# Kernel tuning notes

Hardware: AMD Instinct MI355X
Metric: run time of the kernel (lower is better)

The kernel has to match this reference:

```python
import jax, jax.numpy as jnp
import numpy as np

ITERATIONS = 3
EPS = 1e-06

def squash(s):
    # square_norm along last dim, keepdims (matches torch squash)
    sq = jnp.sum(s * s, axis=-1, keepdims=True)
    return sq / (1.0 + sq) * s / (jnp.sqrt(sq) + EPS)

def setup_inputs() -> dict:
    key = jax.random.key(0)
    k1, k2 = jax.random.split(key)
    x = jax.random.normal(k1, (64, 32, 8, 8, 16), dtype=jnp.float32)
    W = jax.random.normal(k2, (1, 32, 8, 8, 32, 16, 32), dtype=jnp.float32)
    return {"x": x, "W": W}

def reference(x, W):
    # u_hat: (B, C, H, Wd, O, D) = x (B,C,H,Wd,I) @ W (C,H,Wd,O,I,D)
    u_hat = jnp.einsum('bchwi,chwoid->bchwod', x, W[0])
    b = jnp.zeros(u_hat.shape[:-1], dtype=u_hat.dtype)  # (B,C,H,Wd,O)
    for _ in range(ITERATIONS - 1):
        c = jax.nn.softmax(b, axis=-1)
        s = jnp.sum(c[..., None] * u_hat, axis=(1, 2, 3))  # (B,O,D)
        v = squash(s)
        b = b + jnp.sum(u_hat * v[:, None, None, None], axis=-1)
    c = jax.nn.softmax(b, axis=-1)
    s = jnp.sum(c[..., None] * u_hat, axis=(1, 2, 3))
    return squash(s)  # (B, out_capsules, out_cap_dim)
```

## Files before the change

kernel.cpp:

```cpp
#include <hip/hip_runtime.h>
#include <math.h>

#define B_ 64
#define N_ 2048
#define O_ 32
#define I_ 16
#define D_ 32
#define OD_ 1024

typedef __attribute__((ext_vector_type(8))) short bf16x8;
typedef __attribute__((ext_vector_type(4))) float f32x4;

union FragU { unsigned u[4]; uint4 v; bf16x8 f; };

__device__ __forceinline__ void barrier_lds() {
  asm volatile("s_waitcnt lgkmcnt(0)\n\ts_barrier" ::: "memory");
}

template <int CTRL>
__device__ __forceinline__ float dpp_mov_f(float x) {
  return __int_as_float(
      __builtin_amdgcn_update_dpp(0, __float_as_int(x), CTRL, 0xf, 0xf, true));
}
__device__ __forceinline__ float grp32_max(float x) {
  x = fmaxf(x, dpp_mov_f<0xb1>(x));
  x = fmaxf(x, dpp_mov_f<0x4e>(x));
  x = fmaxf(x, dpp_mov_f<0x124>(x));
  x = fmaxf(x, dpp_mov_f<0x128>(x));
  x = fmaxf(x, __shfl_xor(x, 16));
  return x;
}
__device__ __forceinline__ float grp32_sum(float x) {
  x += dpp_mov_f<0xb1>(x);
  x += dpp_mov_f<0x4e>(x);
  x += dpp_mov_f<0x124>(x);
  x += dpp_mov_f<0x128>(x);
  x += __shfl_xor(x, 16);
  return x;
}

__device__ __forceinline__ void dk_split(float f, unsigned &h, unsigned &l) {
  unsigned u = __float_as_uint(f);
  h = u & 0xffff0000u;
  float lo = f - __uint_as_float(h);
  l = __float_as_uint(lo) >> 16;
}
__device__ __forceinline__ void dk_split16(float f, unsigned short &h,
                                           unsigned short &l) {
  unsigned u = __float_as_uint(f);
  unsigned hu = u & 0xffff0000u;
  h = (unsigned short)(u >> 16);
  float lo = f - __uint_as_float(hu);
  l = (unsigned short)(__float_as_uint(lo) >> 16);
}
__device__ __forceinline__ unsigned pk(unsigned short e0, unsigned short e1) {
  return (unsigned)e0 | ((unsigned)e1 << 16);
}

__global__ __launch_bounds__(256) void prep_all(const float* __restrict__ W,
                                                const float* __restrict__ x,
                                                uint4* __restrict__ WP,
                                                uint4* __restrict__ XP) {
  __shared__ float tile[8 * 512];
  const int tid = threadIdx.x;
  if (blockIdx.x < 8192) {
    const int pair0 = blockIdx.x * 8;
    const f32x4* gsrc = (const f32x4*)(W + (size_t)pair0 * 512);
    f32x4* lds4 = (f32x4*)tile;
#pragma unroll
    for (int k = 0; k < 4; ++k)
      lds4[tid + k * 256] = __builtin_nontemporal_load(gsrc + tid + k * 256);
    __syncthreads();
    const int p = tid >> 5;
    const int d = tid & 31;
    const int pair = pair0 + p;
    unsigned short hh[I_], ll[I_];
#pragma unroll
    for (int i = 0; i < I_; ++i)
      dk_split16(tile[p * 512 + i * 32 + d], hh[i], ll[i]);
    const int c = d & 15, dhalf = d >> 4;
    size_t base = ((size_t)pair * 2 + dhalf) * 4;
#pragma unroll
    for (int sel = 0; sel < 2; ++sel) {
      const unsigned short* e = sel ? ll : hh;
#pragma unroll
      for (int qp = 0; qp < 2; ++qp) {
        uint4 u;
        u.x = pk(e[qp * 8 + 0], e[qp * 8 + 1]);
        u.y = pk(e[qp * 8 + 2], e[qp * 8 + 3]);
        u.z = pk(e[qp * 8 + 4], e[qp * 8 + 5]);
        u.w = pk(e[qp * 8 + 6], e[qp * 8 + 7]);
        WP[(base + sel * 2 + qp) * 16 + c] = u;
      }
    }
  } else {
    int t = (blockIdx.x - 8192) * 256 + tid;
    int c = t & 15, n = (t >> 4) & 2047, bg = t >> 15;
    const f32x4* xq = (const f32x4*)(x + ((size_t)(bg * 16 + c) * N_ + n) * I_);
    float xv[I_];
#pragma unroll
    for (int k = 0; k < 4; ++k) {
      f32x4 q4 = __builtin_nontemporal_load(xq + k);
      xv[4 * k + 0] = q4[0];
      xv[4 * k + 1] = q4[1];
      xv[4 * k + 2] = q4[2];
      xv[4 * k + 3] = q4[3];
    }
    unsigned short hh[I_], ll[I_];
#pragma unroll
    for (int i = 0; i < I_; ++i) dk_split16(xv[i], hh[i], ll[i]);
    size_t base = ((size_t)bg * N_ + n) * 4;
#pragma unroll
    for (int sel = 0; sel < 2; ++sel) {
      const unsigned short* e = sel ? ll : hh;
#pragma unroll
      for (int qp = 0; qp < 2; ++qp) {
        uint4 u;
        u.x = pk(e[qp * 8 + 0], e[qp * 8 + 1]);
        u.y = pk(e[qp * 8 + 2], e[qp * 8 + 3]);
        u.z = pk(e[qp * 8 + 4], e[qp * 8 + 5]);
        u.w = pk(e[qp * 8 + 6], e[qp * 8 + 7]);
        XP[(base + sel * 2 + qp) * 16 + c] = u;
      }
    }
  }
}

template <int UNIFORM>
__global__ __launch_bounds__(1024, 4) void mfma_pass6(
    const uint4* __restrict__ XP, const uint4* __restrict__ WP,
    const float* __restrict__ v, float* __restrict__ partial, int NC) {
  const int tid = threadIdx.x;
  const int lane = tid & 63;
  const int w = tid >> 6;
  const int q = lane >> 4;
  const int c = lane & 15;
  const int qp = q & 1;
  const int ch = blockIdx.x;
  const int bgy = blockIdx.y;

  __shared__ uint4 xps[2][16][4][16];
  __shared__ float ls_l[32 * 33];
  __shared__ float ls_c2[32 * 33];

  const int n0 = ch * NC;

  {
    uint4* xf = (uint4*)xps;
    const int total = 2 * NC * 64;
    for (int l = tid; l < total; l += 1024) {
      int bgl = l / (NC * 64);
      int rest = l - bgl * (NC * 64);
      xf[bgl * 1024 + rest] =
          XP[(size_t)(bgy * 2 + bgl) * 131072 + (size_t)n0 * 64 + rest];
    }
  }

  f32x4 s_t[2][4];
#pragma unroll
  for (int bgl = 0; bgl < 2; ++bgl)
#pragma unroll
    for (int ct = 0; ct < 4; ++ct) s_t[bgl][ct] = (f32x4){0.f, 0.f, 0.f, 0.f};

  float vreg[2][4][4];
  if (!UNIFORM) {
#pragma unroll
    for (int bgl = 0; bgl < 2; ++bgl)
#pragma unroll
      for (int ct = 0; ct < 4; ++ct) {
        const float4 vv = *(const float4*)&v[(size_t)(bgy * 32 + bgl * 16 + c) * OD_ +
                                             (2 * w + (ct >> 1)) * 32 +
                                             (ct & 1) * 16 + q * 4];
        vreg[bgl][ct][0] = vv.x;
        vreg[bgl][ct][1] = vv.y;
        vreg[bgl][ct][2] = vv.z;
        vreg[bgl][ct][3] = vv.w;
      }
  }

  barrier_lds();

  const uint4* wbase = WP + (size_t)(2 * w) * 128 + lane;

  FragU cb[4];
#pragma unroll
  for (int ct = 0; ct < 4; ++ct)
    cb[ct].v = wbase[(size_t)n0 * 4096 + ct * 64];

  if (UNIFORM) {
    for (int nl = 0; nl < NC; ++nl) {
      const size_t n = (size_t)(n0 + nl);
      const size_t np = (nl + 1 < NC) ? n + 1 : n;
      FragU cbn[4];
#pragma unroll
      for (int ct = 0; ct < 4; ++ct) cbn[ct].v = wbase[np * 4096 + ct * 64];
#pragma unroll
      for (int bgl = 0; bgl < 2; ++bgl) {
        FragU ah, al;
        ah.v = xps[bgl][nl][qp][c];
        al.v = xps[bgl][nl][2 + qp][c];
#pragma unroll
        for (int ct = 0; ct < 4; ++ct) {
          s_t[bgl][ct] = __builtin_amdgcn_mfma_f32_16x16x32_bf16(
              ah.f, cb[ct].f, s_t[bgl][ct], 0, 0, 0);
          s_t[bgl][ct] = __builtin_amdgcn_mfma_f32_16x16x32_bf16(
              al.f, cb[ct].f, s_t[bgl][ct], 0, 0, 0);
        }
      }
#pragma unroll
      for (int ct = 0; ct < 4; ++ct) cb[ct] = cbn[ct];
    }
  } else {
    for (int nl = 0; nl < NC; ++nl) {
      const size_t n = (size_t)(n0 + nl);
      const size_t np = (nl + 1 < NC) ? n + 1 : n;

      f32x4 ut[2][4];
#pragma unroll
      for (int bgl = 0; bgl < 2; ++bgl) {
        FragU ah, al;
        ah.v = xps[bgl][nl][qp][c];
        al.v = xps[bgl][nl][2 + qp][c];
        float lgol[2] = {0.f, 0.f};
#pragma unroll
        for (int ct = 0; ct < 4; ++ct) {
          f32x4 accT = (f32x4){0.f, 0.f, 0.f, 0.f};
          accT = __builtin_amdgcn_mfma_f32_16x16x32_bf16(cb[ct].f, ah.f, accT, 0, 0, 0);
          ut[bgl][ct] = __builtin_amdgcn_mfma_f32_16x16x32_bf16(cb[ct].f, al.f, accT, 0, 0, 0);
          const int ol = ct >> 1;
#pragma unroll
          for (int r = 0; r < 4; ++r)
            lgol[ol] = fmaf(ut[bgl][ct][r], vreg[bgl][ct][r], lgol[ol]);
        }
#pragma unroll
        for (int ol = 0; ol < 2; ++ol) {
          float t = lgol[ol];
          t += __shfl_xor(t, 16);
          t += __shfl_xor(t, 32);
          if (q == 0) ls_l[(2 * w + ol) * 33 + bgl * 16 + c] = t;
        }
      }
#pragma unroll
      for (int ct = 0; ct < 4; ++ct) cb[ct].v = wbase[np * 4096 + ct * 64];

      barrier_lds();
      {
        const int idx = (tid & 31) * 33 + (tid >> 5);
        float l = ls_l[idx];
        float mx = grp32_max(l);
        float e = __expf(l - mx);
        float sm = grp32_sum(e);
        ls_c2[idx] = e / sm;
      }
      barrier_lds();
#pragma unroll
      for (int bgl = 0; bgl < 2; ++bgl)
#pragma unroll
        for (int ol = 0; ol < 2; ++ol) {
          const float cc = ls_c2[(2 * w + ol) * 33 + bgl * 16 + c];
#pragma unroll
          for (int dh = 0; dh < 2; ++dh) {
            const int ct = ol * 2 + dh;
#pragma unroll
            for (int r = 0; r < 4; ++r)
              s_t[bgl][ct][r] = fmaf(cc, ut[bgl][ct][r], s_t[bgl][ct][r]);
          }
        }
    }
  }

  if (UNIFORM) {
    const float scale = 1.f / 32.f;
#pragma unroll
    for (int bgl = 0; bgl < 2; ++bgl)
#pragma unroll
      for (int ct = 0; ct < 4; ++ct) {
        int odc = (2 * w + (ct >> 1)) * 32 + (ct & 1) * 16 + c;
#pragma unroll
        for (int r = 0; r < 4; ++r) {
          partial[((size_t)ch * B_ + bgy * 32 + bgl * 16 + q * 4 + r) * OD_ + odc] =
              s_t[bgl][ct][r] * scale;
        }
      }
  } else {
    float* tw = ((float*)xps) + w * 288;
#pragma unroll
    for (int bgl = 0; bgl < 2; ++bgl)
#pragma unroll
      for (int ct = 0; ct < 4; ++ct) {
#pragma unroll
        for (int r = 0; r < 4; ++r) tw[c * 18 + q * 4 + r] = s_t[bgl][ct][r];
        f32x4 so;
#pragma unroll
        for (int r = 0; r < 4; ++r) so[r] = tw[(q * 4 + r) * 18 + c];
        const int odc = (2 * w + (ct >> 1)) * 32 + (ct & 1) * 16 + c;
#pragma unroll
        for (int r = 0; r < 4; ++r) {
          partial[((size_t)ch * B_ + bgy * 32 + bgl * 16 + q * 4 + r) * OD_ + odc] =
              so[r];
        }
      }
  }
}

template <int UNIFORM>
__global__ __launch_bounds__(512, 4) void mfma_pass_fb(
    const float* __restrict__ x, const float* __restrict__ W,
    const float* __restrict__ v, float* __restrict__ partial, int NC) {
  const int tid = threadIdx.x;
  const int lane = tid & 63;
  const int cg = tid >> 6;
  const int q = lane >> 4;
  const int c = lane & 15;
  const int ch = blockIdx.x;
  const int bg = blockIdx.y;

  __shared__ float ls_logit[16 * O_];
  __shared__ float ls_c[16 * O_];

  f32x4 s_t[8];
#pragma unroll
  for (int ct = 0; ct < 8; ++ct) s_t[ct] = (f32x4){0.f, 0.f, 0.f, 0.f};

  const int n0 = ch * NC;
  const int ih = (q & 1) * 8;
  const float* xrow = x + ((size_t)(bg * 16 + c) * N_) * I_ + ih;

  for (int nl = 0; nl < NC; ++nl) {
    const int n = n0 + nl;
    const float* xp = xrow + (size_t)n * I_;
    float4 xv0 = *(const float4*)xp;
    float4 xv1 = *(const float4*)(xp + 4);
    float xv[8] = {xv0.x, xv0.y, xv0.z, xv0.w, xv1.x, xv1.y, xv1.z, xv1.w};
    FragU a1;
#pragma unroll
    for (int p = 0; p < 4; ++p) {
      unsigned h0, l0, h1, l1;
      dk_split(xv[2 * p], h0, l0);
      dk_split(xv[2 * p + 1], h1, l1);
      a1.u[p] = (q < 2) ? ((h0 >> 16) | h1) : (l0 | (l1 << 16));
    }
    f32x4 u_t[8];
#pragma unroll
    for (int ct = 0; ct < 8; ++ct) {
      const int o = cg * 4 + (ct >> 1);
      const int d = (ct & 1) * 16 + c;
      const float* wp = W + (((size_t)n * O_ + o) * I_ + ih) * D_ + d;
      FragU b1, b2;
#pragma unroll
      for (int p = 0; p < 4; ++p) {
        unsigned h0, l0, h1, l1;
        dk_split(wp[(2 * p) * D_], h0, l0);
        dk_split(wp[(2 * p + 1) * D_], h1, l1);
        b1.u[p] = (h0 >> 16) | h1;
        b2.u[p] = l0 | (l1 << 16);
      }
      if (UNIFORM) {
        s_t[ct] = __builtin_amdgcn_mfma_f32_16x16x32_bf16(a1.f, b1.f, s_t[ct], 0, 0, 0);
        s_t[ct] = __builtin_amdgcn_mfma_f32_16x16x32_bf16(a1.f, b2.f, s_t[ct], 0, 0, 0);
      } else {
        f32x4 acc = (f32x4){0.f, 0.f, 0.f, 0.f};
        acc = __builtin_amdgcn_mfma_f32_16x16x32_bf16(a1.f, b1.f, acc, 0, 0, 0);
        u_t[ct] = __builtin_amdgcn_mfma_f32_16x16x32_bf16(a1.f, b2.f, acc, 0, 0, 0);
      }
    }
    if (!UNIFORM) {
#pragma unroll
      for (int ol = 0; ol < 4; ++ol) {
        float lg[4] = {0.f, 0.f, 0.f, 0.f};
#pragma unroll
        for (int hf = 0; hf < 2; ++hf) {
          int ct = ol * 2 + hf;
          int odc = cg * 128 + ct * 16 + c;
#pragma unroll
          for (int r = 0; r < 4; ++r)
            lg[r] = fmaf(u_t[ct][r], v[(size_t)(bg * 16 + q * 4 + r) * OD_ + odc], lg[r]);
        }
#pragma unroll
        for (int r = 0; r < 4; ++r) {
#pragma unroll
          for (int m = 1; m < 16; m <<= 1) lg[r] += __shfl_xor(lg[r], m);
        }
        if (c == 0) {
#pragma unroll
          for (int r = 0; r < 4; ++r)
            ls_logit[(q * 4 + r) * O_ + cg * 4 + ol] = lg[r];
        }
      }
      __syncthreads();
      {
        int b_l = tid >> 5, o = tid & 31;
        float l = ls_logit[b_l * O_ + o];
        float mx = l;
#pragma unroll
        for (int m = 16; m >= 1; m >>= 1) mx = fmaxf(mx, __shfl_xor(mx, m));
        float e = __expf(l - mx);
        float sm = e;
#pragma unroll
        for (int m = 16; m >= 1; m >>= 1) sm += __shfl_xor(sm, m);
        ls_c[b_l * O_ + o] = e / sm;
      }
      __syncthreads();
#pragma unroll
      for (int ol = 0; ol < 4; ++ol) {
        int o = cg * 4 + ol;
        float cc[4];
#pragma unroll
        for (int r = 0; r < 4; ++r) cc[r] = ls_c[(q * 4 + r) * O_ + o];
#pragma unroll
        for (int hf = 0; hf < 2; ++hf) {
          int ct = ol * 2 + hf;
#pragma unroll
          for (int r = 0; r < 4; ++r)
            s_t[ct][r] = fmaf(cc[r], u_t[ct][r], s_t[ct][r]);
        }
      }
    }
  }

  const float scale = UNIFORM ? (1.f / 32.f) : 1.f;
#pragma unroll
  for (int ct = 0; ct < 8; ++ct) {
#pragma unroll
    for (int r = 0; r < 4; ++r) {
      partial[((size_t)ch * B_ + bg * 16 + q * 4 + r) * OD_ + cg * 128 + ct * 16 + c] =
          s_t[ct][r] * scale;
    }
  }
}

__global__ __launch_bounds__(256) void reduce_fused(
    const float4* __restrict__ part, int cq4, const float4* __restrict__ prev,
    float4* __restrict__ out) {
  __shared__ float4 accs[4][64];
  const int lane = threadIdx.x & 63;
  const int cg = threadIdx.x >> 6;
  const int g4 = blockIdx.x * 64 + lane;
  float4 s = make_float4(0.f, 0.f, 0.f, 0.f);
  const int c0 = cg * cq4;
  for (int i = 0; i < cq4; ++i) {
    float4 p = part[(size_t)(c0 + i) * 16384 + g4];
    s.x += p.x; s.y += p.y; s.z += p.z; s.w += p.w;
  }
  accs[cg][lane] = s;
  __syncthreads();
  if (cg == 0) {
    float4 a1 = accs[1][lane], a2 = accs[2][lane], a3 = accs[3][lane];
    s.x += a1.x + a2.x + a3.x;
    s.y += a1.y + a2.y + a3.y;
    s.z += a1.z + a2.z + a3.z;
    s.w += a1.w + a2.w + a3.w;
    float sq = s.x * s.x + s.y * s.y + s.z * s.z + s.w * s.w;
#pragma unroll
    for (int m = 4; m >= 1; m >>= 1) sq += __shfl_xor(sq, m, 8);
    float scale = sq / ((1.f + sq) * (sqrtf(sq) + 1e-6f));
    float4 r = make_float4(s.x * scale, s.y * scale, s.z * scale, s.w * scale);
    if (prev) {
      float4 p = prev[g4];
      r.x += p.x; r.y += p.y; r.z += p.z; r.w += p.w;
    }
    out[g4] = r;
  }
}

__global__ __launch_bounds__(256) void reduce_squash(
    const float4* __restrict__ part, int chunks,
    const float4* __restrict__ prev, float4* __restrict__ out) {
  int g4 = blockIdx.x * 256 + threadIdx.x;
  float4 s = make_float4(0.f, 0.f, 0.f, 0.f);
#pragma unroll 4
  for (int ch = 0; ch < chunks; ++ch) {
    float4 p = part[(size_t)ch * 16384 + g4];
    s.x += p.x; s.y += p.y; s.z += p.z; s.w += p.w;
  }
  float sq = s.x * s.x + s.y * s.y + s.z * s.z + s.w * s.w;
#pragma unroll
  for (int m = 4; m >= 1; m >>= 1) sq += __shfl_xor(sq, m, 8);
  float scale = sq / ((1.f + sq) * (sqrtf(sq) + 1e-6f));
  float4 r = make_float4(s.x * scale, s.y * scale, s.z * scale, s.w * scale);
  if (prev) {
    float4 p = prev[g4];
    r.x += p.x; r.y += p.y; r.z += p.z; r.w += p.w;
  }
  out[g4] = r;
}

extern "C" void kernel_launch(void* const* d_in, const int* in_sizes, int n_in,
                              void* d_out, int out_size, void* d_ws,
                              size_t ws_size, hipStream_t stream) {
  const float* x = (const float*)d_in[0];
  const float* W = (const float*)d_in[1];
  float* out = (float*)d_out;

  const size_t XP_FLOATS = 4ull * 2048 * 4 * 16 * 4;
  const size_t WP_FLOATS = 2048ull * 32 * 2 * 4 * 16 * 4;

  float* v1 = (float*)d_ws;
  float* vsum = v1 + 65536;
  float* partial = vsum + 65536;

  const int chunks = 128;
  bool packed_path =
      (131072 + (size_t)chunks * 65536 + XP_FLOATS + WP_FLOATS) * 4 <= ws_size;

  if (packed_path) {
    uint4* XP = (uint4*)(partial + (size_t)chunks * 65536);
    uint4* WP = XP + XP_FLOATS / 4;
    const int NC = N_ / chunks;
    const int cq4 = chunks / 4;
    dim3 grid(chunks, 2);

    prep_all<<<8704, 256, 0, stream>>>(W, x, WP, XP);

    mfma_pass6<1><<<grid, 1024, 0, stream>>>(XP, WP, nullptr, partial, NC);
    reduce_fused<<<256, 256, 0, stream>>>((const float4*)partial, cq4, nullptr,
                                          (float4*)v1);
    mfma_pass6<0><<<grid, 1024, 0, stream>>>(XP, WP, v1, partial, NC);
    reduce_fused<<<256, 256, 0, stream>>>((const float4*)partial, cq4,
                                          (const float4*)v1, (float4*)vsum);
    mfma_pass6<0><<<grid, 1024, 0, stream>>>(XP, WP, vsum, partial, NC);
    reduce_fused<<<256, 256, 0, stream>>>((const float4*)partial, cq4, nullptr,
                                          (float4*)out);
  } else {
    int fchunks = 128;
    while (fchunks > 1 && (131072 + (size_t)fchunks * 65536) * 4 > ws_size)
      fchunks >>= 1;
    int NC = N_ / fchunks;
    dim3 grid(fchunks, 4);

    mfma_pass_fb<1><<<grid, 512, 0, stream>>>(x, W, nullptr, partial, NC);
    reduce_squash<<<64, 256, 0, stream>>>((const float4*)partial, fchunks,
                                          nullptr, (float4*)v1);
    mfma_pass_fb<0><<<grid, 512, 0, stream>>>(x, W, v1, partial, NC);
    reduce_squash<<<64, 256, 0, stream>>>((const float4*)partial, fchunks,
                                          (const float4*)v1, (float4*)vsum);
    mfma_pass_fb<0><<<grid, 512, 0, stream>>>(x, W, vsum, partial, NC);
    reduce_squash<<<64, 256, 0, stream>>>((const float4*)partial, fchunks,
                                          nullptr, (float4*)out);
  }
}
```

Before: 355.4 us.

## Split routing pass into uniform kernel and narrower 512-thread non-uniform kernel

Splits the templated pass into a dedicated uniform-routing kernel and a separate non-uniform kernel. In the non-uniform kernel each block now handles one 16-batch group with 512 threads (grid doubled in y), and each wave covers four output capsules instead of two. The v vector is now loaded from global memory every iteration through an opaque offset rather than held in registers, which lowers register pressure. The aim is more blocks and smaller barriers in the softmax-per-step loop. The cost is that each W fragment is fetched twice as often across blocks, plus extra v loads inside the loop.

```diff
diff --git a/kernel.cpp b/kernel.cpp
--- a/kernel.cpp
+++ b/kernel.cpp
@@ -126,8 +126,84 @@
   }
 }
 
-template <int UNIFORM>
-__global__ __launch_bounds__(1024, 4) void mfma_pass6(
+__global__ __launch_bounds__(1024, 4) void mfma_pass_u(
+    const uint4* __restrict__ XP, const uint4* __restrict__ WP,
+    float* __restrict__ partial, int NC) {
+  const int tid = threadIdx.x;
+  const int lane = tid & 63;
+  const int w = tid >> 6;
+  const int q = lane >> 4;
+  const int c = lane & 15;
+  const int qp = q & 1;
+  const int ch = blockIdx.x;
+  const int bgy = blockIdx.y;
+
+  __shared__ uint4 xps[2][16][4][16];
+
+  const int n0 = ch * NC;
+  {
+    uint4* xf = (uint4*)xps;
+    const int total = 2 * NC * 64;
+    for (int l = tid; l < total; l += 1024) {
+      int bgl = l / (NC * 64);
+      int rest = l - bgl * (NC * 64);
+      xf[bgl * 1024 + rest] =
+          XP[(size_t)(bgy * 2 + bgl) * 131072 + (size_t)n0 * 64 + rest];
+    }
+  }
+
+  f32x4 s_t[2][4];
+#pragma unroll
+  for (int bgl = 0; bgl < 2; ++bgl)
+#pragma unroll
+    for (int ct = 0; ct < 4; ++ct) s_t[bgl][ct] = (f32x4){0.f, 0.f, 0.f, 0.f};
+
+  barrier_lds();
+
+  const uint4* wbase = WP + (size_t)(2 * w) * 128 + lane;
+  FragU cb[4];
+#pragma unroll
+  for (int ct = 0; ct < 4; ++ct)
+    cb[ct].v = wbase[(size_t)n0 * 4096 + ct * 64];
+
+  for (int nl = 0; nl < NC; ++nl) {
+    const size_t n = (size_t)(n0 + nl);
+    const size_t np = (nl + 1 < NC) ? n + 1 : n;
+    FragU cbn[4];
+#pragma unroll
+    for (int ct = 0; ct < 4; ++ct) cbn[ct].v = wbase[np * 4096 + ct * 64];
+#pragma unroll
+    for (int bgl = 0; bgl < 2; ++bgl) {
+      FragU ah, al;
+      ah.v = xps[bgl][nl][qp][c];
+      al.v = xps[bgl][nl][2 + qp][c];
+#pragma unroll
+      for (int ct = 0; ct < 4; ++ct) {
+        s_t[bgl][ct] = __builtin_amdgcn_mfma_f32_16x16x32_bf16(
+            ah.f, cb[ct].f, s_t[bgl][ct], 0, 0, 0);
+        s_t[bgl][ct] = __builtin_amdgcn_mfma_f32_16x16x32_bf16(
+            al.f, cb[ct].f, s_t[bgl][ct], 0, 0, 0);
+      }
+    }
+#pragma unroll
+    for (int ct = 0; ct < 4; ++ct) cb[ct] = cbn[ct];
+  }
+
+  const float scale = 1.f / 32.f;
+#pragma unroll
+  for (int bgl = 0; bgl < 2; ++bgl)
+#pragma unroll
+    for (int ct = 0; ct < 4; ++ct) {
+      int odc = (2 * w + (ct >> 1)) * 32 + (ct & 1) * 16 + c;
+#pragma unroll
+      for (int r = 0; r < 4; ++r) {
+        partial[((size_t)ch * B_ + bgy * 32 + bgl * 16 + q * 4 + r) * OD_ + odc] =
+            s_t[bgl][ct][r] * scale;
+      }
+    }
+}
+
+__global__ __launch_bounds__(512, 4) void mfma_passN(
     const uint4* __restrict__ XP, const uint4* __restrict__ WP,
     const float* __restrict__ v, float* __restrict__ partial, int NC) {
   const int tid = threadIdx.x;
@@ -139,167 +215,106 @@
   const int ch = blockIdx.x;
   const int bgy = blockIdx.y;
 
-  __shared__ uint4 xps[2][16][4][16];
-  __shared__ float ls_l[32 * 33];
-  __shared__ float ls_c2[32 * 33];
+  __shared__ uint4 xps[16][4][16];
+  __shared__ float ls_l[32 * 17];
+  __shared__ float ls_c2[32 * 17];
 
   const int n0 = ch * NC;
 
   {
     uint4* xf = (uint4*)xps;
-    const int total = 2 * NC * 64;
-    for (int l = tid; l < total; l += 1024) {
-      int bgl = l / (NC * 64);
-      int rest = l - bgl * (NC * 64);
-      xf[bgl * 1024 + rest] =
-          XP[(size_t)(bgy * 2 + bgl) * 131072 + (size_t)n0 * 64 + rest];
-    }
-  }
-
-  f32x4 s_t[2][4];
-#pragma unroll
-  for (int bgl = 0; bgl < 2; ++bgl)
-#pragma unroll
-    for (int ct = 0; ct < 4; ++ct) s_t[bgl][ct] = (f32x4){0.f, 0.f, 0.f, 0.f};
-
-  float vreg[2][4][4];
-  if (!UNIFORM) {
-#pragma unroll
-    for (int bgl = 0; bgl < 2; ++bgl)
-#pragma unroll
-      for (int ct = 0; ct < 4; ++ct) {
-        const float4 vv = *(const float4*)&v[(size_t)(bgy * 32 + bgl * 16 + c) * OD_ +
-                                             (2 * w + (ct >> 1)) * 32 +
-                                             (ct & 1) * 16 + q * 4];
-        vreg[bgl][ct][0] = vv.x;
-        vreg[bgl][ct][1] = vv.y;
-        vreg[bgl][ct][2] = vv.z;
-        vreg[bgl][ct][3] = vv.w;
-      }
-  }
+    const int total = NC * 64;
+    for (int l = tid; l < total; l += 512)
+      xf[l] = XP[(size_t)bgy * 131072 + (size_t)n0 * 64 + l];
+  }
+
+  f32x4 s_t[8];
+#pragma unroll
+  for (int ct = 0; ct < 8; ++ct) s_t[ct] = (f32x4){0.f, 0.f, 0.f, 0.f};
 
   barrier_lds();
 
-  const uint4* wbase = WP + (size_t)(2 * w) * 128 + lane;
-
-  FragU cb[4];
-#pragma unroll
-  for (int ct = 0; ct < 4; ++ct)
-    cb[ct].v = wbase[(size_t)n0 * 4096 + ct * 64];
-
-  if (UNIFORM) {
-    for (int nl = 0; nl < NC; ++nl) {
-      const size_t n = (size_t)(n0 + nl);
-      const size_t np = (nl + 1 < NC) ? n + 1 : n;
-      FragU cbn[4];
-#pragma unroll
-      for (int ct = 0; ct < 4; ++ct) cbn[ct].v = wbase[np * 4096 + ct * 64];
-#pragma unroll
-      for (int bgl = 0; bgl < 2; ++bgl) {
-        FragU ah, al;
-        ah.v = xps[bgl][nl][qp][c];
-        al.v = xps[bgl][nl][2 + qp][c];
-#pragma unroll
-        for (int ct = 0; ct < 4; ++ct) {
-          s_t[bgl][ct] = __builtin_amdgcn_mfma_f32_16x16x32_bf16(
-              ah.f, cb[ct].f, s_t[bgl][ct], 0, 0, 0);
-          s_t[bgl][ct] = __builtin_amdgcn_mfma_f32_16x16x32_bf16(
-              al.f, cb[ct].f, s_t[bgl][ct], 0, 0, 0);
-        }
-      }
-#pragma unroll
-      for (int ct = 0; ct < 4; ++ct) cb[ct] = cbn[ct];
-    }
-  } else {
-    for (int nl = 0; nl < NC; ++nl) {
-      const size_t n = (size_t)(n0 + nl);
-      const size_t np = (nl + 1 < NC) ? n + 1 : n;
-
-      f32x4 ut[2][4];
-#pragma unroll
-      for (int bgl = 0; bgl < 2; ++bgl) {
-        FragU ah, al;
-        ah.v = xps[bgl][nl][qp][c];
-        al.v = xps[bgl][nl][2 + qp][c];
-        float lgol[2] = {0.f, 0.f};
-#pragma unroll
-        for (int ct = 0; ct < 4; ++ct) {
-          f32x4 accT = (f32x4){0.f, 0.f, 0.f, 0.f};
-          accT = __builtin_amdgcn_mfma_f32_16x16x32_bf16(cb[ct].f, ah.f, accT, 0, 0, 0);
-          ut[bgl][ct] = __builtin_amdgcn_mfma_f32_16x16x32_bf16(cb[ct].f, al.f, accT, 0, 0, 0);
-          const int ol = ct >> 1;
-#pragma unroll
-          for (int r = 0; r < 4; ++r)
-            lgol[ol] = fmaf(ut[bgl][ct][r], vreg[bgl][ct][r], lgol[ol]);
-        }
-#pragma unroll
-        for (int ol = 0; ol < 2; ++ol) {
-          float t = lgol[ol];
-          t += __shfl_xor(t, 16);
-          t += __shfl_xor(t, 32);
-          if (q == 0) ls_l[(2 * w + ol) * 33 + bgl * 16 + c] = t;
-        }
-      }
-#pragma unroll
-      for (int ct = 0; ct < 4; ++ct) cb[ct].v = wbase[np * 4096 + ct * 64];
-
-      barrier_lds();
-      {
-        const int idx = (tid & 31) * 33 + (tid >> 5);
-        float l = ls_l[idx];
-        float mx = grp32_max(l);
-        float e = __expf(l - mx);
-        float sm = grp32_sum(e);
-        ls_c2[idx] = e / sm;
-      }
-      barrier_lds();
-#pragma unroll
-      for (int bgl = 0; bgl < 2; ++bgl)
-#pragma unroll
-        for (int ol = 0; ol < 2; ++ol) {
-          const float cc = ls_c2[(2 * w + ol) * 33 + bgl * 16 + c];
-#pragma unroll
-          for (int dh = 0; dh < 2; ++dh) {
-            const int ct = ol * 2 + dh;
-#pragma unroll
-            for (int r = 0; r < 4; ++r)
-              s_t[bgl][ct][r] = fmaf(cc, ut[bgl][ct][r], s_t[bgl][ct][r]);
-          }
-        }
-    }
-  }
-
-  if (UNIFORM) {
-    const float scale = 1.f / 32.f;
-#pragma unroll
-    for (int bgl = 0; bgl < 2; ++bgl)
-#pragma unroll
-      for (int ct = 0; ct < 4; ++ct) {
-        int odc = (2 * w + (ct >> 1)) * 32 + (ct & 1) * 16 + c;
-#pragma unroll
-        for (int r = 0; r < 4; ++r) {
-          partial[((size_t)ch * B_ + bgy * 32 + bgl * 16 + q * 4 + r) * OD_ + odc] =
-              s_t[bgl][ct][r] * scale;
-        }
-      }
-  } else {
-    float* tw = ((float*)xps) + w * 288;
-#pragma unroll
-    for (int bgl = 0; bgl < 2; ++bgl)
-#pragma unroll
-      for (int ct = 0; ct < 4; ++ct) {
-#pragma unroll
-        for (int r = 0; r < 4; ++r) tw[c * 18 + q * 4 + r] = s_t[bgl][ct][r];
-        f32x4 so;
-#pragma unroll
-        for (int r = 0; r < 4; ++r) so[r] = tw[(q * 4 + r) * 18 + c];
-        const int odc = (2 * w + (ct >> 1)) * 32 + (ct & 1) * 16 + c;
-#pragma unroll
-        for (int r = 0; r < 4; ++r) {
-          partial[((size_t)ch * B_ + bgy * 32 + bgl * 16 + q * 4 + r) * OD_ + odc] =
-              so[r];
-        }
-      }
+  const uint4* wbase = WP + (size_t)(4 * w) * 128 + lane;
+  FragU cb[8];
+#pragma unroll
+  for (int ct = 0; ct < 8; ++ct)
+    cb[ct].v = wbase[(size_t)n0 * 4096 + (ct >> 1) * 128 + (ct & 1) * 64];
+
+  int zero = 0;
+  const size_t vrow = (size_t)(bgy * 16 + c) * OD_ + (4 * w) * 32 + q * 4;
+
+  for (int nl = 0; nl < NC; ++nl) {
+    const size_t n = (size_t)(n0 + nl);
+    const size_t np = (nl + 1 < NC) ? n + 1 : n;
+
+    asm volatile("" : "+v"(zero));
+    const float* vp = v + vrow + zero;
+
+    f32x4 ut[8];
+    FragU ah, al;
+    ah.v = xps[nl][qp][c];
+    al.v = xps[nl][2 + qp][c];
+    float lgol[4] = {0.f, 0.f, 0.f, 0.f};
+#pragma unroll
+    for (int ct = 0; ct < 8; ++ct) {
+      f32x4 accT = (f32x4){0.f, 0.f, 0.f, 0.f};
+      accT = __builtin_amdgcn_mfma_f32_16x16x32_bf16(cb[ct].f, ah.f, accT, 0, 0, 0);
+      ut[ct] = __builtin_amdgcn_mfma_f32_16x16x32_bf16(cb[ct].f, al.f, accT, 0, 0, 0);
+      const float4 vv =
+          *(const float4*)(vp + (ct >> 1) * 32 + (ct & 1) * 16);
+      const int ol = ct >> 1;
+      lgol[ol] = fmaf(ut[ct][0], vv.x, lgol[ol]);
+      lgol[ol] = fmaf(ut[ct][1], vv.y, lgol[ol]);
+      lgol[ol] = fmaf(ut[ct][2], vv.z, lgol[ol]);
+      lgol[ol] = fmaf(ut[ct][3], vv.w, lgol[ol]);
+    }
+#pragma unroll
+    for (int ol = 0; ol < 4; ++ol) {
+      float t = lgol[ol];
+      t += __shfl_xor(t, 16);
+      t += __shfl_xor(t, 32);
+      if (q == 0) ls_l[(4 * w + ol) * 17 + c] = t;
+    }
+#pragma unroll
+    for (int ct = 0; ct < 8; ++ct)
+      cb[ct].v = wbase[np * 4096 + (ct >> 1) * 128 + (ct & 1) * 64];
+
+    barrier_lds();
+    {
+      const int idx = (tid & 31) * 17 + (tid >> 5);
+      float l = ls_l[idx];
+      float mx = grp32_max(l);
+      float e = __expf(l - mx);
+      float sm = grp32_sum(e);
+      ls_c2[idx] = e / sm;
+    }
+    barrier_lds();
+#pragma unroll
+    for (int ol = 0; ol < 4; ++ol) {
+      const float cc = ls_c2[(4 * w + ol) * 17 + c];
+#pragma unroll
+      for (int dh = 0; dh < 2; ++dh) {
+        const int ct = ol * 2 + dh;
+#pragma unroll
+        for (int r = 0; r < 4; ++r)
+          s_t[ct][r] = fmaf(cc, ut[ct][r], s_t[ct][r]);
+      }
+    }
+  }
+
+  float* tw = ((float*)xps) + w * 288;
+#pragma unroll
+  for (int ct = 0; ct < 8; ++ct) {
+#pragma unroll
+    for (int r = 0; r < 4; ++r) tw[c * 18 + q * 4 + r] = s_t[ct][r];
+    f32x4 so;
+#pragma unroll
+    for (int r = 0; r < 4; ++r) so[r] = tw[(q * 4 + r) * 18 + c];
+    const int odc = (4 * w + (ct >> 1)) * 32 + (ct & 1) * 16 + c;
+#pragma unroll
+    for (int r = 0; r < 4; ++r) {
+      partial[((size_t)ch * B_ + bgy * 16 + q * 4 + r) * OD_ + odc] = so[r];
+    }
   }
 }
 
@@ -508,17 +523,16 @@
     uint4* WP = XP + XP_FLOATS / 4;
     const int NC = N_ / chunks;
     const int cq4 = chunks / 4;
-    dim3 grid(chunks, 2);
 
     prep_all<<<8704, 256, 0, stream>>>(W, x, WP, XP);
 
-    mfma_pass6<1><<<grid, 1024, 0, stream>>>(XP, WP, nullptr, partial, NC);
+    mfma_pass_u<<<dim3(chunks, 2), 1024, 0, stream>>>(XP, WP, partial, NC);
     reduce_fused<<<256, 256, 0, stream>>>((const float4*)partial, cq4, nullptr,
                                           (float4*)v1);
-    mfma_pass6<0><<<grid, 1024, 0, stream>>>(XP, WP, v1, partial, NC);
+    mfma_passN<<<dim3(chunks, 4), 512, 0, stream>>>(XP, WP, v1, partial, NC);
     reduce_fused<<<256, 256, 0, stream>>>((const float4*)partial, cq4,
                                           (const float4*)v1, (float4*)vsum);
-    mfma_pass6<0><<<grid, 1024, 0, stream>>>(XP, WP, vsum, partial, NC);
+    mfma_passN<<<dim3(chunks, 4), 512, 0, stream>>>(XP, WP, vsum, partial, NC);
     reduce_fused<<<256, 256, 0, stream>>>((const float4*)partial, cq4, nullptr,
                                           (float4*)out);
   } else {
```

Measured after the change: 418.6 us. 1.18x slower.
